# Kernel tuning notes

Measured on AMD Instinct MI355X. Metric: run time of the kernel, lower is better.

Reference implementation:

```python
import jax, jax.numpy as jnp
import numpy as np

N = 100000      # num nodes
E = 1600000     # num edges (avg degree 16)
F_IN = 700      # hardcoded in_feats in build()
H = 128         # args.hidden
EPS = 1e-5      # BatchNorm1d eps


def setup_inputs() -> dict:
    key = jax.random.key(0)
    ks = jax.random.split(key, 12)
    w = lambda k, shape: jax.random.normal(k, shape, dtype=jnp.float32) * 0.05
    return {
        "inputs": jax.random.normal(ks[0], (1, N, F_IN), dtype=jnp.float32),
        "graph": jax.random.randint(ks[1], (1, E, 2), 0, N, dtype=jnp.int32),
        "Wself0": w(ks[2], (F_IN, H)),
        "Wneigh0": w(ks[3], (F_IN, H)),
        "b0": jnp.zeros((H,), jnp.float32),
        "Wself": w(ks[4], (3, H, H)),
        "Wneigh": w(ks[5], (3, H, H)),
        "b": jnp.zeros((3, H), jnp.float32),
        "bn_gamma": jnp.ones((4, H), jnp.float32),
        "bn_beta": jnp.zeros((4, H), jnp.float32),
        "W1": w(ks[6], (H, 64)),
        "b1": jnp.zeros((64,), jnp.float32),
        "bng1": jnp.ones((64,), jnp.float32),
        "bnb1": jnp.zeros((64,), jnp.float32),
        "W2": w(ks[7], (64, 1)),
        "b2": jnp.zeros((1,), jnp.float32),
    }


def _batch_norm(x, g, beta):
    # training-mode BN over node dim (biased variance, as PyTorch normalizes)
    mu = jnp.mean(x, axis=0)
    var = jnp.mean((x - mu) ** 2, axis=0)
    return (x - mu) * jax.lax.rsqrt(var + EPS) * g + beta


def reference(inputs, graph, Wself0, Wneigh0, b0, Wself, Wneigh, b,
              bn_gamma, bn_beta, W1, b1, bng1, bnb1, W2, b2):
    h = inputs[0]                      # [N, F_IN] (squeeze + flatten is a no-op)
    edges = graph[0]                   # [E, 2]
    src, dst = edges[:, 0], edges[:, 1]
    deg = jax.ops.segment_sum(jnp.ones((E,), jnp.float32), dst, num_segments=N)
    denom = jnp.maximum(deg, 1.0)[:, None]   # DGL clamps zero in-degree

    def sage(x, Ws, Wn, bias):
        # SAGEConv(mean): fc before message passing (linearity => equivalent)
        hn = x @ Wn                                                   # [N, H]
        agg = jax.ops.segment_sum(hn[src], dst, num_segments=N) / denom
        return x @ Ws + agg + bias

    # layer 0: no residual
    h = sage(h, Wself0, Wneigh0, b0)
    h = jax.nn.relu(_batch_norm(h, bn_gamma[0], bn_beta[0]))
    # layers 1..3: BN + residual + relu (dropout = identity in eval)
    for l in range(3):
        pre = h
        h = sage(h, Wself[l], Wneigh[l], b[l])
        h = _batch_norm(h, bn_gamma[l + 1], bn_beta[l + 1])
        h = jax.nn.relu(h + pre)

    z = _batch_norm(h @ W1 + b1, bng1, bnb1)
    z = jax.nn.relu(z)
    out = z @ W2 + b2                  # [N, 1]
    return out.T                       # permute(1,0) -> [1, N]
```

## Files before the change

kernel.cpp:

```cpp
#include <hip/hip_runtime.h>
#include <hip/hip_bf16.h>

#define N_NODES 100000
#define N_EDGES 1600000
#define F_IN    700
#define NKB0    22
#define HDIM    128
#define SCAN_B  256
#define NB_SCAN ((N_NODES + SCAN_B - 1) / SCAN_B)

typedef _Float16 half8 __attribute__((ext_vector_type(8)));
typedef _Float16 half4 __attribute__((ext_vector_type(4)));
typedef float floatx4 __attribute__((ext_vector_type(4)));

__device__ __forceinline__ void cp16(const void* g, void* l) {
    __builtin_amdgcn_global_load_lds(
        (const __attribute__((address_space(1))) void*)g,
        (__attribute__((address_space(3))) void*)l, 16, 0, 0);
}

__global__ void count_edges(const int* __restrict__ graph, int* __restrict__ cnt) {
    int e = blockIdx.x * blockDim.x + threadIdx.x;
    if (e < N_EDGES) atomicAdd(&cnt[graph[2 * e + 1]], 1);
}

__global__ void scan1(const int* __restrict__ cnt, int* __restrict__ incl,
                      int* __restrict__ blk) {
    __shared__ int s[SCAN_B];
    int tid = threadIdx.x;
    int i = blockIdx.x * SCAN_B + tid;
    s[tid] = (i < N_NODES) ? cnt[i] : 0;
    __syncthreads();
    for (int off = 1; off < SCAN_B; off <<= 1) {
        int t = (tid >= off) ? s[tid - off] : 0;
        __syncthreads();
        s[tid] += t;
        __syncthreads();
    }
    if (i < N_NODES) incl[i] = s[tid];
    if (tid == SCAN_B - 1) blk[blockIdx.x] = s[tid];
}

__global__ void scan2(const int* __restrict__ blk, int* __restrict__ blkoff) {
    __shared__ int s[512];
    int tid = threadIdx.x;
    s[tid] = (tid < NB_SCAN) ? blk[tid] : 0;
    __syncthreads();
    for (int off = 1; off < 512; off <<= 1) {
        int t = (tid >= off) ? s[tid - off] : 0;
        __syncthreads();
        s[tid] += t;
        __syncthreads();
    }
    if (tid < NB_SCAN) blkoff[tid] = (tid == 0) ? 0 : s[tid - 1];
}

__global__ void scan3(const int* __restrict__ incl, const int* __restrict__ blkoff,
                      int* __restrict__ row_ptr) {
    int i = blockIdx.x * SCAN_B + threadIdx.x;
    if (i < N_NODES) {
        row_ptr[i + 1] = incl[i] + blkoff[i >> 8];
        if (i == 0) row_ptr[0] = 0;
    }
}

__global__ void fill_edges(const int* __restrict__ graph, const int* __restrict__ row_ptr,
                           int* __restrict__ cursor, int* __restrict__ esrc) {
    int e = blockIdx.x * blockDim.x + threadIdx.x;
    if (e < N_EDGES) {
        int src = graph[2 * e];
        int dst = graph[2 * e + 1];
        esrc[row_ptr[dst] + atomicAdd(&cursor[dst], 1)] = src;
    }
}

__global__ void build_wtp0(const float* __restrict__ Wn, const float* __restrict__ Ws,
                           _Float16* __restrict__ out) {
    int q = blockIdx.x * blockDim.x + threadIdx.x;
    if (q >= NKB0 * 256 * 4) return;
    int kb = q >> 10;
    int r  = (q >> 2) & 255;
    int cc = q & 3;
    int k0 = kb * 32 + (cc ^ ((r >> 1) & 3)) * 8;
    half8 v;
    #pragma unroll
    for (int e = 0; e < 8; e++) {
        int k = k0 + e;
        float f = 0.0f;
        if (k < F_IN) f = (r < 128) ? Wn[k * 128 + r] : Ws[k * 128 + (r - 128)];
        v[e] = (_Float16)f;
    }
    *(half8*)&out[(size_t)q * 8] = v;
}

__global__ void build_wtpl(const float* __restrict__ Wn, const float* __restrict__ Ws,
                           _Float16* __restrict__ out) {
    int q = blockIdx.x * blockDim.x + threadIdx.x;
    if (q >= 3 * 4 * 256 * 4) return;
    int l = q >> 12;
    int rem = q & 4095;
    int kb = rem >> 10;
    int r  = (rem >> 2) & 255;
    int cc = rem & 3;
    int k0 = kb * 32 + (cc ^ ((r >> 1) & 3)) * 8;
    half8 v;
    #pragma unroll
    for (int e = 0; e < 8; e++) {
        int k = k0 + e;
        float f = (r < 128) ? Wn[l * 16384 + k * 128 + r]
                            : Ws[l * 16384 + k * 128 + (r - 128)];
        v[e] = (_Float16)f;
    }
    *(half8*)&out[(size_t)q * 8] = v;
}

__global__ __launch_bounds__(256) void gemm0_ns(
    const float* __restrict__ A, int M, int K,
    const _Float16* __restrict__ Wtp, const float* __restrict__ bias,
    const float* __restrict__ zbuf,
    _Float16* __restrict__ Cn, float* __restrict__ Cs) {
    __shared__ char sbuf[2][24576];

    int tid = threadIdx.x;
    int wave = tid >> 6, lane = tid & 63;
    int lm = lane & 15, quad = lane >> 4;
    int wm = wave >> 1, wn = wave & 1;
    int bx = blockIdx.x;
    long row0 = (long)(bx >> 1) * 128;
    int nh = bx & 1;

    floatx4 acc[4][4] = {};

    auto stage = [&](int kb, char* buf) {
        #pragma unroll
        for (int pass = 0; pass < 4; pass++) {
            int q = pass * 256 + tid;
            int r = q >> 3, cc = q & 7;
            int ccg = cc ^ (r & 7);
            long grow = row0 + r;
            int gk = kb * 32 + ccg * 4;
            const float* src = (gk + 4 <= K) ? (A + grow * (long)K + gk) : zbuf;
            char* dst = buf + pass * 4096 + wave * 1024;
            if (grow < M) cp16(src, dst);
        }
        const _Float16* wsrc = Wtp + (size_t)kb * 8192 + nh * 4096;
        #pragma unroll
        for (int pass = 0; pass < 2; pass++) {
            cp16(wsrc + (size_t)(pass * 256 + tid) * 8,
                 buf + 16384 + pass * 4096 + wave * 1024);
        }
    };

    stage(0, sbuf[0]);
    __syncthreads();

    for (int kb = 0; kb < NKB0; kb++) {
        int p = kb & 1;
        if (kb + 1 < NKB0) stage(kb + 1, sbuf[p ^ 1]);

        const float* Af = (const float*)sbuf[p];
        const _Float16* Bf = (const _Float16*)(sbuf[p] + 16384);
        half8 af[4];
        #pragma unroll
        for (int i = 0; i < 4; i++) {
            int row = wm * 64 + i * 16 + lm;
            int c0 = (quad * 2) ^ (row & 7);
            int c1 = (quad * 2 + 1) ^ (row & 7);
            floatx4 f0 = *(const floatx4*)&Af[row * 32 + c0 * 4];
            floatx4 f1 = *(const floatx4*)&Af[row * 32 + c1 * 4];
            af[i][0] = (_Float16)f0[0]; af[i][1] = (_Float16)f0[1];
            af[i][2] = (_Float16)f0[2]; af[i][3] = (_Float16)f0[3];
            af[i][4] = (_Float16)f1[0]; af[i][5] = (_Float16)f1[1];
            af[i][6] = (_Float16)f1[2]; af[i][7] = (_Float16)f1[3];
        }
        #pragma unroll
        for (int j = 0; j < 4; j++) {
            int brow = wn * 64 + j * 16 + lm;
            int ch = quad ^ ((brow >> 1) & 3);
            half8 bf = *(const half8*)&Bf[brow * 32 + ch * 8];
            #pragma unroll
            for (int i = 0; i < 4; i++)
                acc[i][j] = __builtin_amdgcn_mfma_f32_16x16x32_f16(af[i], bf, acc[i][j], 0, 0, 0);
        }
        __syncthreads();
    }

    #pragma unroll
    for (int i = 0; i < 4; i++) {
        long r0 = row0 + wm * 64 + i * 16 + quad * 4;
        #pragma unroll
        for (int j = 0; j < 4; j++) {
            int c = wn * 64 + j * 16 + lm;
            if (nh) {
                float badd = bias[c];
                #pragma unroll
                for (int rr = 0; rr < 4; rr++) {
                    long r = r0 + rr;
                    if (r < M) Cs[r * HDIM + c] = acc[i][j][rr] + badd;
                }
            } else {
                #pragma unroll
                for (int rr = 0; rr < 4; rr++) {
                    long r = r0 + rr;
                    if (r < M) Cn[r * HDIM + c] = (_Float16)acc[i][j][rr];
                }
            }
        }
    }
}

__global__ __launch_bounds__(256) void gemm16_ns(
    const _Float16* __restrict__ A, int M,
    const _Float16* __restrict__ Wtp, const float* __restrict__ bias,
    _Float16* __restrict__ Cn, float* __restrict__ Cs) {
    __shared__ _Float16 sbuf[2][8192];

    int tid = threadIdx.x;
    int wave = tid >> 6, lane = tid & 63;
    int lm = lane & 15, quad = lane >> 4;
    int wm = wave >> 1, wn = wave & 1;
    int bx = blockIdx.x;
    long row0 = (long)(bx >> 1) * 128;
    int nh = bx & 1;

    floatx4 acc[4][4] = {};

    auto stage = [&](int kb, _Float16* buf) {
        #pragma unroll
        for (int pass = 0; pass < 2; pass++) {
            int q = pass * 256 + tid;
            int r = q >> 2, cc = q & 3;
            int ccg = cc ^ ((r >> 1) & 3);
            long grow = row0 + r;
            _Float16* dst = buf + pass * 2048 + wave * 512;
            if (grow < M)
                cp16(A + grow * (long)HDIM + kb * 32 + ccg * 8, dst);
        }
        const _Float16* wsrc = Wtp + (size_t)kb * 8192 + nh * 4096;
        #pragma unroll
        for (int pass = 0; pass < 2; pass++) {
            cp16(wsrc + (size_t)(pass * 256 + tid) * 8,
                 buf + 4096 + pass * 2048 + wave * 512);
        }
    };

    stage(0, sbuf[0]);
    __syncthreads();

    for (int kb = 0; kb < 4; kb++) {
        int p = kb & 1;
        if (kb + 1 < 4) stage(kb + 1, sbuf[p ^ 1]);

        const _Float16* bp = sbuf[p];
        half8 af[4];
        #pragma unroll
        for (int i = 0; i < 4; i++) {
            int row = wm * 64 + i * 16 + lm;
            int ch = quad ^ ((row >> 1) & 3);
            af[i] = *(const half8*)&bp[row * 32 + ch * 8];
        }
        #pragma unroll
        for (int j = 0; j < 4; j++) {
            int brow = wn * 64 + j * 16 + lm;
            int ch = quad ^ ((brow >> 1) & 3);
            half8 bf = *(const half8*)&bp[4096 + brow * 32 + ch * 8];
            #pragma unroll
            for (int i = 0; i < 4; i++)
                acc[i][j] = __builtin_amdgcn_mfma_f32_16x16x32_f16(af[i], bf, acc[i][j], 0, 0, 0);
        }
        __syncthreads();
    }

    #pragma unroll
    for (int i = 0; i < 4; i++) {
        long r0 = row0 + wm * 64 + i * 16 + quad * 4;
        #pragma unroll
        for (int j = 0; j < 4; j++) {
            int c = wn * 64 + j * 16 + lm;
            if (nh) {
                float badd = bias[c];
                #pragma unroll
                for (int rr = 0; rr < 4; rr++) {
                    long r = r0 + rr;
                    if (r < M) Cs[r * HDIM + c] = acc[i][j][rr] + badd;
                }
            } else {
                #pragma unroll
                for (int rr = 0; rr < 4; rr++) {
                    long r = r0 + rr;
                    if (r < M) Cn[r * HDIM + c] = (_Float16)acc[i][j][rr];
                }
            }
        }
    }
}

__global__ __launch_bounds__(256) void aggregate_w(
    const _Float16* __restrict__ hn, const int* __restrict__ row_ptr,
    const int* __restrict__ esrc, float* __restrict__ pre) {
    int wave = threadIdx.x >> 6, lane = threadIdx.x & 63;
    int n = blockIdx.x * 4 + wave;
    if (n >= N_NODES) return;
    int start = row_ptr[n], end = row_ptr[n + 1];
    int eg = lane >> 4;
    int c8 = (lane & 15) * 8;

    float acc[8] = {};
    for (int base = start; base < end; base += 16) {
        #pragma unroll
        for (int u = 0; u < 4; u++) {
            int e = base + u * 4 + eg;
            if (e < end) {
                int s = esrc[e];
                half8 v = *(const half8*)&hn[(size_t)s * HDIM + c8];
                #pragma unroll
                for (int i = 0; i < 8; i++) acc[i] += (float)v[i];
            }
        }
    }
    #pragma unroll
    for (int i = 0; i < 8; i++) {
        acc[i] += __shfl_xor(acc[i], 16, 64);
        acc[i] += __shfl_xor(acc[i], 32, 64);
    }
    if (eg == 0) {
        float rd = 1.0f / (float)max(end - start, 1);
        size_t off = (size_t)n * HDIM + c8;
        float4 p0 = *(float4*)&pre[off];
        float4 p1 = *(float4*)&pre[off + 4];
        p0.x += acc[0] * rd; p0.y += acc[1] * rd;
        p0.z += acc[2] * rd; p0.w += acc[3] * rd;
        p1.x += acc[4] * rd; p1.y += acc[5] * rd;
        p1.z += acc[6] * rd; p1.w += acc[7] * rd;
        *(float4*)&pre[off]     = p0;
        *(float4*)&pre[off + 4] = p1;
    }
}

__global__ void bn_stats(const float* __restrict__ P, float* __restrict__ gsum,
                         float* __restrict__ gsumsq, int M, int C) {
    int tid = threadIdx.x;
    int c = tid % C;
    int rpb = 256 / C;
    float s = 0.0f, s2 = 0.0f;
    for (int r = blockIdx.x * rpb + tid / C; r < M; r += gridDim.x * rpb) {
        float v = P[(size_t)r * C + c];
        s += v; s2 += v * v;
    }
    __shared__ float ss[256], ss2[256];
    ss[tid] = s; ss2[tid] = s2;
    __syncthreads();
    for (int off = 128; off >= C; off >>= 1) {
        if (tid < off) { ss[tid] += ss[tid + off]; ss2[tid] += ss2[tid + off]; }
        __syncthreads();
    }
    if (tid < C) {
        atomicAdd(&gsum[tid], ss[tid]);
        atomicAdd(&gsumsq[tid], ss2[tid]);
    }
}

__global__ void bn_apply16(const float* __restrict__ P, const _Float16* __restrict__ res16,
                           _Float16* __restrict__ out16,
                           const float* __restrict__ gsum, const float* __restrict__ gsumsq,
                           const float* __restrict__ gamma, const float* __restrict__ beta,
                           int M, int total4, int Cdiv4) {
    __shared__ float ssc[HDIM], ssh[HDIM];
    int tid = threadIdx.x;
    int C = Cdiv4 * 4;
    if (tid < C) {
        float mean = gsum[tid] / (float)M;
        float var = gsumsq[tid] / (float)M - mean * mean;
        float sc = rsqrtf(var + 1e-5f) * gamma[tid];
        ssc[tid] = sc;
        ssh[tid] = beta[tid] - mean * sc;
    }
    __syncthreads();
    for (int f = blockIdx.x * blockDim.x + tid; f < total4;
         f += gridDim.x * blockDim.x) {
        int c4 = (f % Cdiv4) * 4;
        float4 v = ((const float4*)P)[f];
        v.x = v.x * ssc[c4 + 0] + ssh[c4 + 0];
        v.y = v.y * ssc[c4 + 1] + ssh[c4 + 1];
        v.z = v.z * ssc[c4 + 2] + ssh[c4 + 2];
        v.w = v.w * ssc[c4 + 3] + ssh[c4 + 3];
        if (res16) {
            half4 rv = *(const half4*)&res16[(size_t)f * 4];
            v.x += (float)rv[0]; v.y += (float)rv[1];
            v.z += (float)rv[2]; v.w += (float)rv[3];
        }
        half4 h;
        h[0] = (_Float16)fmaxf(v.x, 0.0f); h[1] = (_Float16)fmaxf(v.y, 0.0f);
        h[2] = (_Float16)fmaxf(v.z, 0.0f); h[3] = (_Float16)fmaxf(v.w, 0.0f);
        *(half4*)&out16[(size_t)f * 4] = h;
    }
}

__global__ __launch_bounds__(256) void mlp_gemm(const _Float16* __restrict__ H,
                                                const float* __restrict__ W1,
                                                const float* __restrict__ b1,
                                                float* __restrict__ Z, int M) {
    __shared__ float hs[64 * 132];
    __shared__ float ws[128 * 64];
    int tid = threadIdx.x;
    int tx = tid & 15;
    int ty = tid >> 4;
    int row0 = blockIdx.x * 64;

    #pragma unroll
    for (int t = 0; t < 8; t++) {
        int f = tid + t * 256;
        int r = f >> 4, c4 = (f & 15) * 4;
        *(float4*)&ws[r * 64 + c4] = *(const float4*)&W1[r * 64 + c4];
    }
    #pragma unroll
    for (int t = 0; t < 4; t++) {
        int f = tid + t * 256;
        int r = f >> 4, c8 = (f & 15) * 8;
        int gr = row0 + r;
        if (gr < M) {
            half8 hv = *(const half8*)&H[(size_t)gr * HDIM + c8];
            #pragma unroll
            for (int i = 0; i < 8; i++) hs[r * 132 + c8 + i] = (float)hv[i];
        } else {
            #pragma unroll
            for (int i = 0; i < 8; i++) hs[r * 132 + c8 + i] = 0.0f;
        }
    }
    __syncthreads();

    float acc[4][4] = {};
    for (int k = 0; k < 128; k++) {
        float a[4];
        #pragma unroll
        for (int i = 0; i < 4; i++) a[i] = hs[(ty * 4 + i) * 132 + k];
        float4 b4 = *(const float4*)&ws[k * 64 + tx * 4];
        #pragma unroll
        for (int i = 0; i < 4; i++) {
            acc[i][0] += a[i] * b4.x; acc[i][1] += a[i] * b4.y;
            acc[i][2] += a[i] * b4.z; acc[i][3] += a[i] * b4.w;
        }
    }
    float4 bb = *(const float4*)&b1[tx * 4];
    #pragma unroll
    for (int i = 0; i < 4; i++) {
        int r = row0 + ty * 4 + i;
        if (r < M) {
            float4 v = {acc[i][0] + bb.x, acc[i][1] + bb.y,
                        acc[i][2] + bb.z, acc[i][3] + bb.w};
            *(float4*)&Z[(size_t)r * 64 + tx * 4] = v;
        }
    }
}

__global__ void final_out(const float* __restrict__ Z,
                          const float* __restrict__ gsum, const float* __restrict__ gsumsq,
                          const float* __restrict__ gamma, const float* __restrict__ beta,
                          const float* __restrict__ W2, const float* __restrict__ b2,
                          float* __restrict__ out, int M) {
    __shared__ float ssc[64], ssh[64], sw[64];
    int tid = threadIdx.x;
    if (tid < 64) {
        float mean = gsum[tid] / (float)M;
        float var = gsumsq[tid] / (float)M - mean * mean;
        float sc = rsqrtf(var + 1e-5f) * gamma[tid];
        ssc[tid] = sc;
        ssh[tid] = beta[tid] - mean * sc;
        sw[tid] = W2[tid];
    }
    __syncthreads();
    int n = blockIdx.x * 4 + (tid >> 6);
    int lane = tid & 63;
    if (n >= N_NODES) return;
    float z = Z[(size_t)n * 64 + lane] * ssc[lane] + ssh[lane];
    z = fmaxf(z, 0.0f);
    float v = z * sw[lane];
    #pragma unroll
    for (int off = 32; off >= 1; off >>= 1) v += __shfl_down(v, off, 64);
    if (lane == 0) out[n] = v + b2[0];
}

extern "C" void kernel_launch(void* const* d_in, const int* in_sizes, int n_in,
                              void* d_out, int out_size, void* d_ws, size_t ws_size,
                              hipStream_t stream) {
    const float* X       = (const float*)d_in[0];
    const int*   graph   = (const int*)d_in[1];
    const float* Wself0  = (const float*)d_in[2];
    const float* Wneigh0 = (const float*)d_in[3];
    const float* b0      = (const float*)d_in[4];
    const float* Wself   = (const float*)d_in[5];
    const float* Wneigh  = (const float*)d_in[6];
    const float* bvec    = (const float*)d_in[7];
    const float* bn_g    = (const float*)d_in[8];
    const float* bn_b    = (const float*)d_in[9];
    const float* W1      = (const float*)d_in[10];
    const float* b1      = (const float*)d_in[11];
    const float* bng1    = (const float*)d_in[12];
    const float* bnb1    = (const float*)d_in[13];
    const float* W2      = (const float*)d_in[14];
    const float* b2      = (const float*)d_in[15];
    float* out = (float*)d_out;

    size_t off = 0;
    auto alloc = [&](size_t bytes) {
        void* p = (char*)d_ws + off;
        off += (bytes + 255) & ~(size_t)255;
        return p;
    };
    int* cnt     = (int*)alloc(N_NODES * 4);
    int* cursor  = (int*)alloc(N_NODES * 4);
    int* row_ptr = (int*)alloc((N_NODES + 1) * 4);
    int* incl    = (int*)alloc(N_NODES * 4);
    int* blk     = (int*)alloc(NB_SCAN * 4);
    int* blkoff  = (int*)alloc(NB_SCAN * 4);
    int* esrc    = (int*)alloc((size_t)N_EDGES * 4);
    float*    pre   = (float*)alloc((size_t)N_NODES * HDIM * 4);
    _Float16* h16A  = (_Float16*)alloc((size_t)N_NODES * HDIM * 2);
    _Float16* h16B  = (_Float16*)alloc((size_t)N_NODES * HDIM * 2);
    _Float16* hn16  = (_Float16*)alloc((size_t)N_NODES * HDIM * 2);
    float*    Z     = (float*)alloc((size_t)N_NODES * 64 * 4);
    _Float16* Wtp0  = (_Float16*)alloc((size_t)NKB0 * 8192 * 2);
    _Float16* Wtpl  = (_Float16*)alloc((size_t)3 * 4 * 8192 * 2);
    float*    zbuf  = (float*)alloc(256);
    float* stats = (float*)alloc(256 * 4);
    float* gsum = stats, *gsumsq = stats + 128;

    const int EB = (N_EDGES + 255) / 256;
    const int GB = ((N_NODES + 127) / 128) * 2;
    const int AGB = (N_NODES + 3) / 4;

    hipMemsetAsync(cnt, 0, N_NODES * 4, stream);
    hipMemsetAsync(cursor, 0, N_NODES * 4, stream);
    hipMemsetAsync(zbuf, 0, 256, stream);
    count_edges<<<EB, 256, 0, stream>>>(graph, cnt);
    scan1<<<NB_SCAN, SCAN_B, 0, stream>>>(cnt, incl, blk);
    scan2<<<1, 512, 0, stream>>>(blk, blkoff);
    scan3<<<NB_SCAN, SCAN_B, 0, stream>>>(incl, blkoff, row_ptr);
    fill_edges<<<EB, 256, 0, stream>>>(graph, row_ptr, cursor, esrc);

    build_wtp0<<<(NKB0 * 1024 + 255) / 256, 256, 0, stream>>>(Wneigh0, Wself0, Wtp0);
    build_wtpl<<<(3 * 4096 + 255) / 256, 256, 0, stream>>>(Wneigh, Wself, Wtpl);

    _Float16* hc = h16A;
    _Float16* hx = h16B;

    gemm0_ns<<<GB, 256, 0, stream>>>(X, N_NODES, F_IN, Wtp0, b0, zbuf, hn16, pre);
    aggregate_w<<<AGB, 256, 0, stream>>>(hn16, row_ptr, esrc, pre);
    hipMemsetAsync(stats, 0, 256 * 4, stream);
    bn_stats<<<512, 256, 0, stream>>>(pre, gsum, gsumsq, N_NODES, 128);
    bn_apply16<<<1024, 256, 0, stream>>>(pre, nullptr, hc, gsum, gsumsq,
                                         bn_g, bn_b, N_NODES,
                                         N_NODES * HDIM / 4, HDIM / 4);

    for (int l = 0; l < 3; l++) {
        gemm16_ns<<<GB, 256, 0, stream>>>(hc, N_NODES, Wtpl + (size_t)l * 32768,
                                          bvec + l * HDIM, hn16, pre);
        aggregate_w<<<AGB, 256, 0, stream>>>(hn16, row_ptr, esrc, pre);
        hipMemsetAsync(stats, 0, 256 * 4, stream);
        bn_stats<<<512, 256, 0, stream>>>(pre, gsum, gsumsq, N_NODES, 128);
        bn_apply16<<<1024, 256, 0, stream>>>(pre, hc, hx, gsum, gsumsq,
                                             bn_g + (l + 1) * HDIM,
                                             bn_b + (l + 1) * HDIM, N_NODES,
                                             N_NODES * HDIM / 4, HDIM / 4);
        _Float16* t = hc; hc = hx; hx = t;
    }

    mlp_gemm<<<(N_NODES + 63) / 64, 256, 0, stream>>>(hc, W1, b1, Z, N_NODES);
    hipMemsetAsync(stats, 0, 256 * 4, stream);
    bn_stats<<<512, 256, 0, stream>>>(Z, gsum, gsumsq, N_NODES, 64);
    final_out<<<AGB, 256, 0, stream>>>(Z, gsum, gsumsq, bng1, bnb1, W2, b2,
                                       out, N_NODES);
}
```

Before: 1.328 ms.

## Replace LDS-staged GEMMs with direct global-to-register MFMA operand loads

Both node GEMMs drop LDS double buffering through global_load_lds and instead load A rows and transposed weight rows straight into registers in MFMA fragment layout, with one k-step of register prefetch. Weight pre-packing becomes a plain transpose to row-major [256][K] fp16. The aim is to remove LDS traffic and the per-k-step barriers. In exchange, operands are no longer shared through LDS, so each wave issues its own strided global loads and relies on the cache for reuse across the four waves, which raises global load instruction count and register pressure.

Result: slower. 1.501 ms (+13.0%).

```diff
diff --git a/kernel.cpp b/kernel.cpp
--- a/kernel.cpp
+++ b/kernel.cpp
@@ -4,6 +4,7 @@
 #define N_NODES 100000
 #define N_EDGES 1600000
 #define F_IN    700
+#define KROW    704
 #define NKB0    22
 #define HDIM    128
 #define SCAN_B  256
@@ -12,12 +13,6 @@
 typedef _Float16 half8 __attribute__((ext_vector_type(8)));
 typedef _Float16 half4 __attribute__((ext_vector_type(4)));
 typedef float floatx4 __attribute__((ext_vector_type(4)));
-
-__device__ __forceinline__ void cp16(const void* g, void* l) {
-    __builtin_amdgcn_global_load_lds(
-        (const __attribute__((address_space(1))) void*)g,
-        (__attribute__((address_space(3))) void*)l, 16, 0, 0);
-}
 
 __global__ void count_edges(const int* __restrict__ graph, int* __restrict__ cnt) {
     int e = blockIdx.x * blockDim.x + threadIdx.x;
@@ -74,53 +69,33 @@
     }
 }
 
-__global__ void build_wtp0(const float* __restrict__ Wn, const float* __restrict__ Ws,
-                           _Float16* __restrict__ out) {
-    int q = blockIdx.x * blockDim.x + threadIdx.x;
-    if (q >= NKB0 * 256 * 4) return;
-    int kb = q >> 10;
-    int r  = (q >> 2) & 255;
-    int cc = q & 3;
-    int k0 = kb * 32 + (cc ^ ((r >> 1) & 3)) * 8;
-    half8 v;
-    #pragma unroll
-    for (int e = 0; e < 8; e++) {
-        int k = k0 + e;
-        float f = 0.0f;
-        if (k < F_IN) f = (r < 128) ? Wn[k * 128 + r] : Ws[k * 128 + (r - 128)];
-        v[e] = (_Float16)f;
-    }
-    *(half8*)&out[(size_t)q * 8] = v;
-}
-
-__global__ void build_wtpl(const float* __restrict__ Wn, const float* __restrict__ Ws,
-                           _Float16* __restrict__ out) {
-    int q = blockIdx.x * blockDim.x + threadIdx.x;
-    if (q >= 3 * 4 * 256 * 4) return;
-    int l = q >> 12;
-    int rem = q & 4095;
-    int kb = rem >> 10;
-    int r  = (rem >> 2) & 255;
-    int cc = rem & 3;
-    int k0 = kb * 32 + (cc ^ ((r >> 1) & 3)) * 8;
-    half8 v;
-    #pragma unroll
-    for (int e = 0; e < 8; e++) {
-        int k = k0 + e;
-        float f = (r < 128) ? Wn[l * 16384 + k * 128 + r]
-                            : Ws[l * 16384 + k * 128 + (r - 128)];
-        v[e] = (_Float16)f;
-    }
-    *(half8*)&out[(size_t)q * 8] = v;
-}
-
-__global__ __launch_bounds__(256) void gemm0_ns(
-    const float* __restrict__ A, int M, int K,
-    const _Float16* __restrict__ Wtp, const float* __restrict__ bias,
+__global__ void build_wt0(const float* __restrict__ Wn, const float* __restrict__ Ws,
+                          _Float16* __restrict__ out) {
+    int idx = blockIdx.x * blockDim.x + threadIdx.x;
+    if (idx >= 256 * KROW) return;
+    int n = idx / KROW, k = idx % KROW;
+    float v = 0.0f;
+    if (k < F_IN) v = (n < 128) ? Wn[k * 128 + n] : Ws[k * 128 + (n - 128)];
+    out[idx] = (_Float16)v;
+}
+
+__global__ void build_wtl(const float* __restrict__ Wn, const float* __restrict__ Ws,
+                          _Float16* __restrict__ out) {
+    int idx = blockIdx.x * blockDim.x + threadIdx.x;
+    if (idx >= 3 * 256 * 128) return;
+    int l = idx / (256 * 128);
+    int rem = idx % (256 * 128);
+    int n = rem / 128, k = rem % 128;
+    float v = (n < 128) ? Wn[l * 16384 + k * 128 + n]
+                        : Ws[l * 16384 + k * 128 + (n - 128)];
+    out[idx] = (_Float16)v;
+}
+
+__global__ __launch_bounds__(256) void gemm0_reg(
+    const float* __restrict__ A, int M,
+    const _Float16* __restrict__ Wt, const float* __restrict__ bias,
     const float* __restrict__ zbuf,
     _Float16* __restrict__ Cn, float* __restrict__ Cs) {
-    __shared__ char sbuf[2][24576];
-
     int tid = threadIdx.x;
     int wave = tid >> 6, lane = tid & 63;
     int lm = lane & 15, quad = lane >> 4;
@@ -129,60 +104,67 @@
     long row0 = (long)(bx >> 1) * 128;
     int nh = bx & 1;
 
+    const float* ap[4];
+    bool rv[4];
+    #pragma unroll
+    for (int i = 0; i < 4; i++) {
+        long r = row0 + wm * 64 + i * 16 + lm;
+        rv[i] = (r < M);
+        ap[i] = A + (rv[i] ? r : 0) * (long)F_IN;
+    }
+    const _Float16* bp[4];
+    #pragma unroll
+    for (int j = 0; j < 4; j++) {
+        int brow = nh * 128 + wn * 64 + j * 16 + lm;
+        bp[j] = Wt + (size_t)brow * KROW;
+    }
+
     floatx4 acc[4][4] = {};
-
-    auto stage = [&](int kb, char* buf) {
-        #pragma unroll
-        for (int pass = 0; pass < 4; pass++) {
-            int q = pass * 256 + tid;
-            int r = q >> 3, cc = q & 7;
-            int ccg = cc ^ (r & 7);
-            long grow = row0 + r;
-            int gk = kb * 32 + ccg * 4;
-            const float* src = (gk + 4 <= K) ? (A + grow * (long)K + gk) : zbuf;
-            char* dst = buf + pass * 4096 + wave * 1024;
-            if (grow < M) cp16(src, dst);
-        }
-        const _Float16* wsrc = Wtp + (size_t)kb * 8192 + nh * 4096;
-        #pragma unroll
-        for (int pass = 0; pass < 2; pass++) {
-            cp16(wsrc + (size_t)(pass * 256 + tid) * 8,
-                 buf + 16384 + pass * 4096 + wave * 1024);
-        }
-    };
-
-    stage(0, sbuf[0]);
-    __syncthreads();
+    floatx4 a0[4], a1[4];
+    half8 bnx[4];
+
+    {
+        int k = quad * 8;
+        #pragma unroll
+        for (int i = 0; i < 4; i++) {
+            const float* s = rv[i] ? (ap[i] + k) : zbuf;
+            a0[i] = *(const floatx4*)s;
+            a1[i] = *(const floatx4*)(rv[i] ? (ap[i] + k + 4) : zbuf);
+        }
+        #pragma unroll
+        for (int j = 0; j < 4; j++) bnx[j] = *(const half8*)(bp[j] + k);
+    }
 
     for (int kb = 0; kb < NKB0; kb++) {
-        int p = kb & 1;
-        if (kb + 1 < NKB0) stage(kb + 1, sbuf[p ^ 1]);
-
-        const float* Af = (const float*)sbuf[p];
-        const _Float16* Bf = (const _Float16*)(sbuf[p] + 16384);
-        half8 af[4];
+        half8 af[4], bf[4];
         #pragma unroll
         for (int i = 0; i < 4; i++) {
-            int row = wm * 64 + i * 16 + lm;
-            int c0 = (quad * 2) ^ (row & 7);
-            int c1 = (quad * 2 + 1) ^ (row & 7);
-            floatx4 f0 = *(const floatx4*)&Af[row * 32 + c0 * 4];
-            floatx4 f1 = *(const floatx4*)&Af[row * 32 + c1 * 4];
-            af[i][0] = (_Float16)f0[0]; af[i][1] = (_Float16)f0[1];
-            af[i][2] = (_Float16)f0[2]; af[i][3] = (_Float16)f0[3];
-            af[i][4] = (_Float16)f1[0]; af[i][5] = (_Float16)f1[1];
-            af[i][6] = (_Float16)f1[2]; af[i][7] = (_Float16)f1[3];
-        }
-        #pragma unroll
-        for (int j = 0; j < 4; j++) {
-            int brow = wn * 64 + j * 16 + lm;
-            int ch = quad ^ ((brow >> 1) & 3);
-            half8 bf = *(const half8*)&Bf[brow * 32 + ch * 8];
+            af[i][0] = (_Float16)a0[i][0]; af[i][1] = (_Float16)a0[i][1];
+            af[i][2] = (_Float16)a0[i][2]; af[i][3] = (_Float16)a0[i][3];
+            af[i][4] = (_Float16)a1[i][0]; af[i][5] = (_Float16)a1[i][1];
+            af[i][6] = (_Float16)a1[i][2]; af[i][7] = (_Float16)a1[i][3];
+        }
+        #pragma unroll
+        for (int j = 0; j < 4; j++) bf[j] = bnx[j];
+
+        if (kb + 1 < NKB0) {
+            int k = (kb + 1) * 32 + quad * 8;
+            bool ok0 = (k + 4 <= F_IN);
+            bool ok1 = (k + 8 <= F_IN);
+            #pragma unroll
+            for (int i = 0; i < 4; i++) {
+                a0[i] = *(const floatx4*)((rv[i] && ok0) ? (ap[i] + k) : zbuf);
+                a1[i] = *(const floatx4*)((rv[i] && ok1) ? (ap[i] + k + 4) : zbuf);
+            }
+            #pragma unroll
+            for (int j = 0; j < 4; j++) bnx[j] = *(const half8*)(bp[j] + k);
+        }
+
+        #pragma unroll
+        for (int j = 0; j < 4; j++)
             #pragma unroll
             for (int i = 0; i < 4; i++)
-                acc[i][j] = __builtin_amdgcn_mfma_f32_16x16x32_f16(af[i], bf, acc[i][j], 0, 0, 0);
-        }
-        __syncthreads();
+                acc[i][j] = __builtin_amdgcn_mfma_f32_16x16x32_f16(af[i], bf[j], acc[i][j], 0, 0, 0);
     }
 
     #pragma unroll
@@ -209,12 +191,11 @@
     }
 }
 
-__global__ __launch_bounds__(256) void gemm16_ns(
+__global__ __launch_bounds__(256) void gemm16_reg(
     const _Float16* __restrict__ A, int M,
-    const _Float16* __restrict__ Wtp, const float* __restrict__ bias,
+    const _Float16* __restrict__ Wt, const float* __restrict__ bias,
+    const _Float16* __restrict__ zbuf16,
     _Float16* __restrict__ Cn, float* __restrict__ Cs) {
-    __shared__ _Float16 sbuf[2][8192];
-
     int tid = threadIdx.x;
     int wave = tid >> 6, lane = tid & 63;
     int lm = lane & 15, quad = lane >> 4;
@@ -223,52 +204,58 @@
     long row0 = (long)(bx >> 1) * 128;
     int nh = bx & 1;
 
+    const _Float16* ap[4];
+    #pragma unroll
+    for (int i = 0; i < 4; i++) {
+        long r = row0 + wm * 64 + i * 16 + lm;
+        ap[i] = (r < M) ? (A + r * (long)HDIM) : zbuf16;
+    }
+    bool rv[4];
+    #pragma unroll
+    for (int i = 0; i < 4; i++) {
+        long r = row0 + wm * 64 + i * 16 + lm;
+        rv[i] = (r < M);
+        ap[i] = A + (rv[i] ? r : 0) * (long)HDIM;
+    }
+    const _Float16* bp[4];
+    #pragma unroll
+    for (int j = 0; j < 4; j++) {
+        int brow = nh * 128 + wn * 64 + j * 16 + lm;
+        bp[j] = Wt + (size_t)brow * HDIM;
+    }
+
     floatx4 acc[4][4] = {};
-
-    auto stage = [&](int kb, _Float16* buf) {
-        #pragma unroll
-        for (int pass = 0; pass < 2; pass++) {
-            int q = pass * 256 + tid;
-            int r = q >> 2, cc = q & 3;
-            int ccg = cc ^ ((r >> 1) & 3);
-            long grow = row0 + r;
-            _Float16* dst = buf + pass * 2048 + wave * 512;
-            if (grow < M)
-                cp16(A + grow * (long)HDIM + kb * 32 + ccg * 8, dst);
-        }
-        const _Float16* wsrc = Wtp + (size_t)kb * 8192 + nh * 4096;
-        #pragma unroll
-        for (int pass = 0; pass < 2; pass++) {
-            cp16(wsrc + (size_t)(pass * 256 + tid) * 8,
-                 buf + 4096 + pass * 2048 + wave * 512);
-        }
-    };
-
-    stage(0, sbuf[0]);
-    __syncthreads();
+    half8 an[4], bnx[4];
+
+    {   int k = quad * 8;
+        #pragma unroll
+        for (int i = 0; i < 4; i++)
+            an[i] = *(const half8*)(rv[i] ? (ap[i] + k) : zbuf16);
+        #pragma unroll
+        for (int j = 0; j < 4; j++) bnx[j] = *(const half8*)(bp[j] + k);
+    }
 
     for (int kb = 0; kb < 4; kb++) {
-        int p = kb & 1;
-        if (kb + 1 < 4) stage(kb + 1, sbuf[p ^ 1]);
-
-        const _Float16* bp = sbuf[p];
-        half8 af[4];
-        #pragma unroll
-        for (int i = 0; i < 4; i++) {
-            int row = wm * 64 + i * 16 + lm;
-            int ch = quad ^ ((row >> 1) & 3);
-            af[i] = *(const half8*)&bp[row * 32 + ch * 8];
-        }
-        #pragma unroll
-        for (int j = 0; j < 4; j++) {
-            int brow = wn * 64 + j * 16 + lm;
-            int ch = quad ^ ((brow >> 1) & 3);
-            half8 bf = *(const half8*)&bp[4096 + brow * 32 + ch * 8];
+        half8 af[4], bf[4];
+        #pragma unroll
+        for (int i = 0; i < 4; i++) af[i] = an[i];
+        #pragma unroll
+        for (int j = 0; j < 4; j++) bf[j] = bnx[j];
+
+        if (kb + 1 < 4) {
+            int k = (kb + 1) * 32 + quad * 8;
             #pragma unroll
             for (int i = 0; i < 4; i++)
-                acc[i][j] = __builtin_amdgcn_mfma_f32_16x16x32_f16(af[i], bf, acc[i][j], 0, 0, 0);
-        }
-        __syncthreads();
+                an[i] = *(const half8*)(rv[i] ? (ap[i] + k) : zbuf16);
+            #pragma unroll
+            for (int j = 0; j < 4; j++) bnx[j] = *(const half8*)(bp[j] + k);
+        }
+
+        #pragma unroll
+        for (int j = 0; j < 4; j++)
+            #pragma unroll
+            for (int i = 0; i < 4; i++)
+                acc[i][j] = __builtin_amdgcn_mfma_f32_16x16x32_f16(af[i], bf[j], acc[i][j], 0, 0, 0);
     }
 
     #pragma unroll
@@ -519,8 +506,8 @@
     _Float16* h16B  = (_Float16*)alloc((size_t)N_NODES * HDIM * 2);
     _Float16* hn16  = (_Float16*)alloc((size_t)N_NODES * HDIM * 2);
     float*    Z     = (float*)alloc((size_t)N_NODES * 64 * 4);
-    _Float16* Wtp0  = (_Float16*)alloc((size_t)NKB0 * 8192 * 2);
-    _Float16* Wtpl  = (_Float16*)alloc((size_t)3 * 4 * 8192 * 2);
+    _Float16* Wt0   = (_Float16*)alloc((size_t)256 * KROW * 2);
+    _Float16* Wtl   = (_Float16*)alloc((size_t)3 * 256 * 128 * 2);
     float*    zbuf  = (float*)alloc(256);
     float* stats = (float*)alloc(256 * 4);
     float* gsum = stats, *gsumsq = stats + 128;
@@ -538,13 +525,13 @@
     scan3<<<NB_SCAN, SCAN_B, 0, stream>>>(incl, blkoff, row_ptr);
     fill_edges<<<EB, 256, 0, stream>>>(graph, row_ptr, cursor, esrc);
 
-    build_wtp0<<<(NKB0 * 1024 + 255) / 256, 256, 0, stream>>>(Wneigh0, Wself0, Wtp0);
-    build_wtpl<<<(3 * 4096 + 255) / 256, 256, 0, stream>>>(Wneigh, Wself, Wtpl);
+    build_wt0<<<(256 * KROW + 255) / 256, 256, 0, stream>>>(Wneigh0, Wself0, Wt0);
+    build_wtl<<<(3 * 256 * 128 + 255) / 256, 256, 0, stream>>>(Wneigh, Wself, Wtl);
 
     _Float16* hc = h16A;
     _Float16* hx = h16B;
 
-    gemm0_ns<<<GB, 256, 0, stream>>>(X, N_NODES, F_IN, Wtp0, b0, zbuf, hn16, pre);
+    gemm0_reg<<<GB, 256, 0, stream>>>(X, N_NODES, Wt0, b0, zbuf, hn16, pre);
     aggregate_w<<<AGB, 256, 0, stream>>>(hn16, row_ptr, esrc, pre);
     hipMemsetAsync(stats, 0, 256 * 4, stream);
     bn_stats<<<512, 256, 0, stream>>>(pre, gsum, gsumsq, N_NODES, 128);
@@ -553,8 +540,9 @@
                                          N_NODES * HDIM / 4, HDIM / 4);
 
     for (int l = 0; l < 3; l++) {
-        gemm16_ns<<<GB, 256, 0, stream>>>(hc, N_NODES, Wtpl + (size_t)l * 32768,
-                                          bvec + l * HDIM, hn16, pre);
+        gemm16_reg<<<GB, 256, 0, stream>>>(hc, N_NODES, Wtl + (size_t)l * 32768,
+                                           bvec + l * HDIM, (const _Float16*)zbuf,
+                                           hn16, pre);
         aggregate_w<<<AGB, 256, 0, stream>>>(hn16, row_ptr, esrc, pre);
         hipMemsetAsync(stats, 0, 256 * 4, stream);
         bn_stats<<<512, 256, 0, stream>>>(pre, gsum, gsumsq, N_NODES, 128);
```
